# Kernel tuning notes

Hardware: AMD Instinct MI355X
Metric: run time of the kernel (lower is better)

## Reference

```python
import jax, jax.numpy as jnp
import numpy as np

N, E, F_IN, F_HID, K = 100000, 1600000, 64, 64, 6


def setup_inputs() -> dict:
    key = jax.random.key(0)
    k1, k2, k3, k4, k5 = jax.random.split(key, 5)
    x = jax.random.normal(k1, (N, F_IN), dtype=jnp.float32)
    # edges with no self-loops (PyG ChebConv removes self loops before normalization)
    src = jax.random.randint(k2, (E,), 0, N, dtype=jnp.int32)
    off = jax.random.randint(k3, (E,), 1, N, dtype=jnp.int32)
    dst = (src + off) % N
    edge_index = jnp.stack([src, dst], axis=0)
    # Glorot-ish init for the K Chebyshev weight matrices
    W = jax.random.normal(k4, (K, F_IN, F_HID), dtype=jnp.float32) * (1.0 / np.sqrt(F_IN))
    b = jax.random.normal(k5, (F_HID,), dtype=jnp.float32) * 0.01
    return {"x": x, "edge_index": edge_index, "W": W, "b": b}


def reference(x, edge_index, W, b):
    # ChebConv with sym normalization, lambda_max = 2.0 (PyG default):
    # scaled Laplacian L_hat = 2*L/lambda_max - I = -D^{-1/2} A D^{-1/2} (zero diagonal)
    row = edge_index[0].astype(jnp.int32)  # source j
    col = edge_index[1].astype(jnp.int32)  # target i
    n = x.shape[0]
    deg = jax.ops.segment_sum(jnp.ones_like(row, dtype=x.dtype), row, num_segments=n)
    dinv = jnp.where(deg > 0, jax.lax.rsqrt(deg), jnp.zeros_like(deg))
    w = -(dinv[row] * dinv[col])  # [E] edge weights of L_hat

    def prop(h):  # h: [N, F] -> L_hat @ h via gather-scale-scatter
        return jax.ops.segment_sum(w[:, None] * h[row], col, num_segments=n)

    # Chebyshev recurrence: Tx_0 = x, Tx_1 = L_hat x, Tx_k = 2 L_hat Tx_{k-1} - Tx_{k-2}
    Tx0 = x
    out = Tx0 @ W[0]
    Tx1 = prop(Tx0)
    out = out + Tx1 @ W[1]
    for k in range(2, W.shape[0]):
        Tx2 = 2.0 * prop(Tx1) - Tx0
        out = out + Tx2 @ W[k]
        Tx0, Tx1 = Tx1, Tx2
    return jax.nn.relu(out + b)
```

## Files before the change

kernel.cpp:

```cpp
#include <hip/hip_runtime.h>


constexpr int F = 64;
constexpr int SCAN_ELEMS = 1024;
constexpr int BSH = 9;
constexpr int EPB = 2048;
constexpr int PNPW = 8;

typedef __attribute__((ext_vector_type(8))) short short8;
typedef __attribute__((ext_vector_type(4))) float floatx4;

__device__ __forceinline__ unsigned short f_to_bf(float f) {
    unsigned u = __float_as_uint(f);
    u += 0x7FFFu + ((u >> 16) & 1u);
    return (unsigned short)(u >> 16);
}
__device__ __forceinline__ float bf_to_f(unsigned short s) {
    return __uint_as_float(((unsigned)s) << 16);
}
__device__ __forceinline__ float4 bf4_to_f4(ushort4 u) {
    float4 f;
    f.x = bf_to_f(u.x); f.y = bf_to_f(u.y); f.z = bf_to_f(u.z); f.w = bf_to_f(u.w);
    return f;
}

__global__ void hist2_kernel(const int* __restrict__ row, const int* __restrict__ col,
                             int* __restrict__ gcH, int* __restrict__ gcS,
                             int P, int G, int E) {
    __shared__ int hH[256], hS[256];
    const int tid = threadIdx.x, blk = blockIdx.x;
    hH[tid] = 0; hS[tid] = 0;
    __syncthreads();
    const int start = blk * EPB + tid * 8;
    if (start + 7 < E) {
        const int4 c0 = *(const int4*)(col + start);
        const int4 c1 = *(const int4*)(col + start + 4);
        const int4 r0 = *(const int4*)(row + start);
        const int4 r1 = *(const int4*)(row + start + 4);
        atomicAdd(&hH[c0.x >> BSH], 1); atomicAdd(&hH[c0.y >> BSH], 1);
        atomicAdd(&hH[c0.z >> BSH], 1); atomicAdd(&hH[c0.w >> BSH], 1);
        atomicAdd(&hH[c1.x >> BSH], 1); atomicAdd(&hH[c1.y >> BSH], 1);
        atomicAdd(&hH[c1.z >> BSH], 1); atomicAdd(&hH[c1.w >> BSH], 1);
        atomicAdd(&hS[r0.x >> BSH], 1); atomicAdd(&hS[r0.y >> BSH], 1);
        atomicAdd(&hS[r0.z >> BSH], 1); atomicAdd(&hS[r0.w >> BSH], 1);
        atomicAdd(&hS[r1.x >> BSH], 1); atomicAdd(&hS[r1.y >> BSH], 1);
        atomicAdd(&hS[r1.z >> BSH], 1); atomicAdd(&hS[r1.w >> BSH], 1);
    } else {
        for (int k = start; k < E && k < start + 8; ++k) {
            atomicAdd(&hH[col[k] >> BSH], 1);
            atomicAdd(&hS[row[k] >> BSH], 1);
        }
    }
    __syncthreads();
    if (tid < P) {
        gcH[(size_t)tid * G + blk] = hH[tid];
        gcS[(size_t)tid * G + blk] = hS[tid];
    }
}

__device__ __forceinline__ int4 load_cnt4(const int* __restrict__ cnt, int i, int N) {
    int4 v = make_int4(0, 0, 0, 0);
    if (i + 3 < N) {
        v = *(const int4*)(cnt + i);
    } else {
        if (i + 0 < N) v.x = cnt[i + 0];
        if (i + 1 < N) v.y = cnt[i + 1];
        if (i + 2 < N) v.z = cnt[i + 2];
        if (i + 3 < N) v.w = cnt[i + 3];
    }
    return v;
}

__global__ void scan1_kernel(const int* __restrict__ cnt, int* __restrict__ bsum, int N) {
    const int tid = threadIdx.x;
    const int i = blockIdx.x * SCAN_ELEMS + tid * 4;
    int4 v = load_cnt4(cnt, i, N);
    int s = v.x + v.y + v.z + v.w;
#pragma unroll
    for (int off = 1; off < 64; off <<= 1) s += __shfl_xor(s, off);
    __shared__ int ws[4];
    if ((tid & 63) == 0) ws[tid >> 6] = s;
    __syncthreads();
    if (tid == 0) bsum[blockIdx.x] = ws[0] + ws[1] + ws[2] + ws[3];
}

__global__ void scan2_kernel(const int* __restrict__ bsum, int* __restrict__ boff,
                             int* __restrict__ total_out, int nb) {
    const int tid = threadIdx.x;
    const int lane = tid & 63, w = tid >> 6;
    int v = (tid < nb) ? bsum[tid] : 0;
    int inc = v;
#pragma unroll
    for (int off = 1; off < 64; off <<= 1) {
        int t = __shfl_up(inc, off);
        if (lane >= off) inc += t;
    }
    __shared__ int wsum[4];
    if (lane == 63) wsum[w] = inc;
    __syncthreads();
    int wo = 0;
    for (int k = 0; k < w; ++k) wo += wsum[k];
    const int excl = wo + inc - v;
    if (tid < nb) boff[tid] = excl;
    if (tid == nb - 1) *total_out = excl + v;
}

__global__ void scan3_kernel(const int* __restrict__ cnt, const int* __restrict__ boff,
                             int* __restrict__ dst, int N) {
    const int tid = threadIdx.x;
    const int lane = tid & 63, w = tid >> 6;
    const int i = blockIdx.x * SCAN_ELEMS + tid * 4;
    int4 v = load_cnt4(cnt, i, N);
    const int s = v.x + v.y + v.z + v.w;
    int inc = s;
#pragma unroll
    for (int off = 1; off < 64; off <<= 1) {
        int t = __shfl_up(inc, off);
        if (lane >= off) inc += t;
    }
    __shared__ int wsum[4];
    if (lane == 63) wsum[w] = inc;
    __syncthreads();
    int wo = 0;
    for (int k = 0; k < w; ++k) wo += wsum[k];
    const int r0 = boff[blockIdx.x] + wo + inc - s;
    const int r1 = r0 + v.x, r2 = r1 + v.y, r3 = r2 + v.z;
    if (i + 3 < N) {
        *(int4*)(dst + i) = make_int4(r0, r1, r2, r3);
    } else {
        if (i + 0 < N) dst[i + 0] = r0;
        if (i + 1 < N) dst[i + 1] = r1;
        if (i + 2 < N) dst[i + 2] = r2;
        if (i + 3 < N) dst[i + 3] = r3;
    }
}

__global__ void part2_kernel(const int* __restrict__ row, const int* __restrict__ col,
                             const int* __restrict__ goH, const int* __restrict__ goS,
                             int2* __restrict__ partH, int* __restrict__ partS,
                             int P, int G, int E) {
    __shared__ int cH[256], cS[256];
    const int tid = threadIdx.x, blk = blockIdx.x;
    if (tid < P) {
        cH[tid] = goH[(size_t)tid * G + blk];
        cS[tid] = goS[(size_t)tid * G + blk];
    }
    __syncthreads();
    const int start = blk * EPB + tid * 8;
    for (int k = start; k < E && k < start + 8; ++k) {
        const int c = col[k], r = row[k];
        const int posH = atomicAdd(&cH[c >> BSH], 1);
        partH[posH] = make_int2(c, r);
        const int posS = atomicAdd(&cS[r >> BSH], 1);
        partS[posS] = r;
    }
}

__global__ void bucketC_kernel(const int2* __restrict__ part, const int* __restrict__ goff,
                               int* __restrict__ rowptr, int* __restrict__ csr,
                               int P, int G, int N, int E) {
    __shared__ int cnt[512];
    __shared__ int excl[512];
    __shared__ int wsum[4];
    const int tid = threadIdx.x;
    const int b = blockIdx.x;
    const int base_node = b << BSH;
    const int nn = min(512, N - base_node);
    const int estart = goff[(size_t)b * G];
    const int eend = (b + 1 < P) ? goff[(size_t)(b + 1) * G] : E;

    cnt[tid] = 0; cnt[tid + 256] = 0;
    __syncthreads();
    for (int i = estart + tid; i < eend; i += 256)
        atomicAdd(&cnt[part[i].x - base_node], 1);
    __syncthreads();
    {
        const int lane = tid & 63, w = tid >> 6;
        const int a0 = cnt[2 * tid], a1 = cnt[2 * tid + 1];
        const int ps = a0 + a1;
        int inc = ps;
#pragma unroll
        for (int off = 1; off < 64; off <<= 1) {
            int t = __shfl_up(inc, off);
            if (lane >= off) inc += t;
        }
        if (lane == 63) wsum[w] = inc;
        __syncthreads();
        int wo = 0;
        for (int k = 0; k < w; ++k) wo += wsum[k];
        const int ep = wo + inc - ps;
        excl[2 * tid] = ep;
        excl[2 * tid + 1] = ep + a0;
    }
    __syncthreads();
    if (tid < nn) rowptr[base_node + tid] = estart + excl[tid];
    for (int ln = 256 + tid; ln < nn; ln += 256) rowptr[base_node + ln] = estart + excl[ln];
    if (b == P - 1 && tid == 0) rowptr[N] = E;
    cnt[tid] = 0; cnt[tid + 256] = 0;
    __syncthreads();
    for (int i = estart + tid; i < eend; i += 256) {
        const int2 e = part[i];
        const int ln = e.x - base_node;
        const int pos = atomicAdd(&cnt[ln], 1);
        csr[estart + excl[ln] + pos] = e.y;
    }
}

__global__ void bucketD_kernel(const int* __restrict__ partS, const int* __restrict__ goffS,
                               float* __restrict__ dinv, float* __restrict__ dinv2,
                               float* __restrict__ rdinv, int P, int G, int N, int E) {
    __shared__ int cnt[512];
    const int tid = threadIdx.x;
    const int b = blockIdx.x;
    const int base_node = b << BSH;
    const int nn = min(512, N - base_node);
    const int estart = goffS[(size_t)b * G];
    const int eend = (b + 1 < P) ? goffS[(size_t)(b + 1) * G] : E;
    cnt[tid] = 0; cnt[tid + 256] = 0;
    __syncthreads();
    for (int i = estart + tid; i < eend; i += 256)
        atomicAdd(&cnt[partS[i] - base_node], 1);
    __syncthreads();
    for (int l = tid; l < nn; l += 256) {
        const int dI = cnt[l];
        const float d = (float)dI;
        const bool ok = dI > 0;
        dinv[base_node + l]  = ok ? rsqrtf(d) : 0.0f;
        dinv2[base_node + l] = ok ? 1.0f / d : 0.0f;
        rdinv[base_node + l] = ok ? sqrtf(d) : 0.0f;
    }
}

__global__ void init_s0_kernel(const float* __restrict__ dinv, const float* __restrict__ x,
                               unsigned short* __restrict__ S0b, int NF) {
    int i = blockIdx.x * blockDim.x + threadIdx.x;
    int j = i * 4;
    if (j >= NF) return;
    const float dv = dinv[j >> 6];
    const float4 v = *(const float4*)(x + j);
    ushort4 u;
    u.x = f_to_bf(dv * v.x); u.y = f_to_bf(dv * v.y);
    u.z = f_to_bf(dv * v.z); u.w = f_to_bf(dv * v.w);
    *(ushort4*)(S0b + j) = u;
}

template <int FIRST>
__global__ __launch_bounds__(256, 8)
void prop_g4(const int* __restrict__ rowptr, const int* __restrict__ csr,
             const float* __restrict__ dinv2, const unsigned short* __restrict__ Sprev,
             const unsigned short* __restrict__ Sm2, unsigned short* __restrict__ Sk, int N) {
    const int lane = threadIdx.x & 63;
    const int g16 = lane & 48;
    const int fl = lane & 15;
    const int wave = threadIdx.x >> 6;
    const int nwaves = blockDim.x >> 6;
    const int wbase = (blockIdx.x * nwaves + wave) * PNPW;
    for (int j = 0; j < PNPW; j += 4) {
        const int n = wbase + j + (g16 >> 4);
        const bool nv = n < N;
        const int nc = nv ? n : N - 1;
        const int s = rowptr[nc];
        const int e = rowptr[nc + 1];
        const int len = e - s;
        float4 acc = {0.f, 0.f, 0.f, 0.f};
        for (int c = 0; c < len; c += 16) {
            const int ii = s + c + fl;
            const int idxv = csr[ii < e ? ii : e - 1];
            const int mm = min(16, len - c);
            for (int jj = 0; jj < mm; jj += 4) {
                const int i0 = __shfl(idxv, g16 + jj + 0);
                const int i1 = __shfl(idxv, g16 + jj + 1);
                const int i2 = __shfl(idxv, g16 + jj + 2);
                const int i3 = __shfl(idxv, g16 + jj + 3);
                const ushort4 u0 = *(const ushort4*)(Sprev + (size_t)i0 * F + fl * 4);
                const ushort4 u1 = *(const ushort4*)(Sprev + (size_t)i1 * F + fl * 4);
                const ushort4 u2 = *(const ushort4*)(Sprev + (size_t)i2 * F + fl * 4);
                const ushort4 u3 = *(const ushort4*)(Sprev + (size_t)i3 * F + fl * 4);
                {
                    const float4 v = bf4_to_f4(u0);
                    acc.x += v.x; acc.y += v.y; acc.z += v.z; acc.w += v.w;
                }
                if (jj + 1 < mm) {
                    const float4 v = bf4_to_f4(u1);
                    acc.x += v.x; acc.y += v.y; acc.z += v.z; acc.w += v.w;
                }
                if (jj + 2 < mm) {
                    const float4 v = bf4_to_f4(u2);
                    acc.x += v.x; acc.y += v.y; acc.z += v.z; acc.w += v.w;
                }
                if (jj + 3 < mm) {
                    const float4 v = bf4_to_f4(u3);
                    acc.x += v.x; acc.y += v.y; acc.z += v.z; acc.w += v.w;
                }
            }
        }
        if (nv) {
            const float d2 = dinv2[n];
            float4 sn;
            if (FIRST) {
                sn.x = -d2 * acc.x; sn.y = -d2 * acc.y;
                sn.z = -d2 * acc.z; sn.w = -d2 * acc.w;
            } else {
                const float4 m2 = bf4_to_f4(*(const ushort4*)(Sm2 + (size_t)n * F + fl * 4));
                sn.x = -2.f * d2 * acc.x - m2.x; sn.y = -2.f * d2 * acc.y - m2.y;
                sn.z = -2.f * d2 * acc.z - m2.z; sn.w = -2.f * d2 * acc.w - m2.w;
            }
            ushort4 o;
            o.x = f_to_bf(sn.x); o.y = f_to_bf(sn.y);
            o.z = f_to_bf(sn.z); o.w = f_to_bf(sn.w);
            *(ushort4*)(Sk + (size_t)n * F + fl * 4) = o;
        }
    }
}

__global__ void wfrag_kernel(const float* __restrict__ W, unsigned short* __restrict__ Wfrag) {
    const int idx = blockIdx.x * blockDim.x + threadIdx.x;
    if (idx >= 4 * 12 * 64) return;
    const int lane = idx & 63;
    const int s = (idx >> 6) % 12;
    const int ft = idx / (64 * 12);
    const int n = ft * 16 + (lane & 15);
    const int quad = lane >> 4;
    unsigned short v[8];
#pragma unroll
    for (int j = 0; j < 8; ++j) {
        const int kg = s * 32 + quad * 8 + j;
        const int kk = kg >> 6, f = kg & 63;
        v[j] = f_to_bf(W[kk * F * F + f * F + n]);
    }
    ushort4 lo = {v[0], v[1], v[2], v[3]};
    ushort4 hi = {v[4], v[5], v[6], v[7]};
    *(ushort4*)(Wfrag + (size_t)idx * 8) = lo;
    *(ushort4*)(Wfrag + (size_t)idx * 8 + 4) = hi;
}

__global__ __launch_bounds__(256, 4)
void mfma_out_kernel(const float* __restrict__ x, const unsigned short* __restrict__ Sstack,
                     const unsigned short* __restrict__ Wfrag, const float* __restrict__ rdinv,
                     const float* __restrict__ dinv2, const float* __restrict__ W,
                     const float* __restrict__ b, float* __restrict__ out, int N, int NF) {
    const int lane = threadIdx.x & 63;
    const int wave = threadIdx.x >> 6;
    const int quad = lane >> 4;
    const int tm = blockIdx.x * 16;
    const int ma = tm + (lane & 15);
    const int mac = ma < N ? ma : N - 1;

    floatx4 C0 = {0.f, 0.f, 0.f, 0.f};
    floatx4 C1 = {0.f, 0.f, 0.f, 0.f};
    const unsigned short* wf = Wfrag + ((size_t)(wave * 12) * 64 + lane) * 8;

    {
        const float* xr = x + (size_t)mac * F + quad * 8;
#pragma unroll
        for (int s = 0; s < 2; ++s) {
            const float4 a0 = *(const float4*)(xr + s * 32);
            const float4 a1 = *(const float4*)(xr + s * 32 + 4);
            short8 A;
            A[0] = (short)f_to_bf(a0.x); A[1] = (short)f_to_bf(a0.y);
            A[2] = (short)f_to_bf(a0.z); A[3] = (short)f_to_bf(a0.w);
            A[4] = (short)f_to_bf(a1.x); A[5] = (short)f_to_bf(a1.y);
            A[6] = (short)f_to_bf(a1.z); A[7] = (short)f_to_bf(a1.w);
            const short8 B = *(const short8*)(wf + (size_t)s * 64 * 8);
            C0 = __builtin_amdgcn_mfma_f32_16x16x32_bf16(A, B, C0, 0, 0, 0);
        }
    }
#pragma unroll
    for (int s = 2; s < 12; ++s) {
        const int kk = s >> 1, f0 = (s & 1) * 32;
        const short8 A = *(const short8*)(Sstack + (size_t)kk * NF + (size_t)mac * F + f0 + quad * 8);
        const short8 B = *(const short8*)(wf + (size_t)s * 64 * 8);
        C1 = __builtin_amdgcn_mfma_f32_16x16x32_bf16(A, B, C1, 0, 0, 0);
    }

    const int n = wave * 16 + (lane & 15);
    const float bl = b[n];
#pragma unroll
    for (int r = 0; r < 4; ++r) {
        const int m = tm + quad * 4 + r;
        if (m >= N) continue;
        float v = C0[r] + rdinv[m] * C1[r];
        if (dinv2[m] == 0.0f) {
            const float* xr = x + (size_t)m * F;
            float fx = 0.f;
            for (int f = 0; f < F; ++f)
                fx += xr[f] * (W[4 * F * F + f * F + n] - W[2 * F * F + f * F + n]);
            v += fx;
        }
        out[(size_t)m * F + n] = fmaxf(v + bl, 0.f);
    }
}

extern "C" void kernel_launch(void* const* d_in, const int* in_sizes, int n_in,
                              void* d_out, int out_size, void* d_ws, size_t ws_size,
                              hipStream_t stream) {
    const float* x = (const float*)d_in[0];
    const int* ei = (const int*)d_in[1];
    const float* W = (const float*)d_in[2];
    const float* b = (const float*)d_in[3];

    const int N = in_sizes[0] / F;
    const int E = in_sizes[1] / 2;
    const int NF = N * F;
    const int* row = ei;
    const int* col = ei + E;

    const int P = (N + 511) >> BSH;
    const int G = (E + EPB - 1) / EPB;
    const int M = P * G;

    char* p = (char*)d_ws;
    auto alloc = [&](size_t bytes) {
        char* r = p;
        p += (bytes + 63) & ~(size_t)63;
        return r;
    };
    float* dinv   = (float*)alloc((size_t)N * sizeof(float));
    float* dinv2  = (float*)alloc((size_t)N * sizeof(float));
    float* rdinv  = (float*)alloc((size_t)N * sizeof(float));
    int*   rowptr = (int*)alloc((size_t)(N + 1) * sizeof(int));
    int*   bsum   = (int*)alloc(256 * sizeof(int));
    int*   boff   = (int*)alloc(256 * sizeof(int));
    int*   totS   = (int*)alloc(64);
    int*   gcH    = (int*)alloc((size_t)M * sizeof(int));
    int*   goH    = (int*)alloc((size_t)M * sizeof(int));
    int*   gcS    = (int*)alloc((size_t)M * sizeof(int));
    int*   goS    = (int*)alloc((size_t)M * sizeof(int));
    int*   csr    = (int*)alloc((size_t)E * sizeof(int));
    unsigned short* Sstack = (unsigned short*)alloc((size_t)6 * NF * sizeof(unsigned short));
    unsigned short* Wfrag  = (unsigned short*)alloc((size_t)4 * 12 * 64 * 8 * sizeof(unsigned short));
    int2* partH = (int2*)Sstack;
    int*  partS = (int*)(Sstack + (size_t)NF);
    float* out = (float*)d_out;

    const int B = 256;
    const int nsbM = (M + SCAN_ELEMS - 1) / SCAN_ELEMS;
    const int pgrid = (N + 4 * PNPW - 1) / (4 * PNPW);

    hist2_kernel<<<G, B, 0, stream>>>(row, col, gcH, gcS, P, G, E);
    scan1_kernel<<<nsbM, B, 0, stream>>>(gcH, bsum, M);
    scan2_kernel<<<1, B, 0, stream>>>(bsum, boff, rowptr + N, nsbM);
    scan3_kernel<<<nsbM, B, 0, stream>>>(gcH, boff, goH, M);
    scan1_kernel<<<nsbM, B, 0, stream>>>(gcS, bsum, M);
    scan2_kernel<<<1, B, 0, stream>>>(bsum, boff, totS, nsbM);
    scan3_kernel<<<nsbM, B, 0, stream>>>(gcS, boff, goS, M);
    part2_kernel<<<G, B, 0, stream>>>(row, col, goH, goS, partH, partS, P, G, E);
    bucketC_kernel<<<P, B, 0, stream>>>(partH, goH, rowptr, csr, P, G, N, E);
    bucketD_kernel<<<P, B, 0, stream>>>(partS, goS, dinv, dinv2, rdinv, P, G, N, E);

    wfrag_kernel<<<(4 * 12 * 64 + B - 1) / B, B, 0, stream>>>(W, Wfrag);
    init_s0_kernel<<<(NF / 4 + B - 1) / B, B, 0, stream>>>(dinv, x, Sstack, NF);
    prop_g4<1><<<pgrid, B, 0, stream>>>(rowptr, csr, dinv2, Sstack, Sstack,
                                        Sstack + (size_t)1 * NF, N);
    for (int k = 2; k < 6; ++k) {
        prop_g4<0><<<pgrid, B, 0, stream>>>(
            rowptr, csr, dinv2, Sstack + (size_t)(k - 1) * NF,
            Sstack + (size_t)(k - 2) * NF, Sstack + (size_t)k * NF, N);
    }
    mfma_out_kernel<<<(N + 15) / 16, 256, 0, stream>>>(x, Sstack, Wfrag, rdinv, dinv2,
                                                       W, b, out, N, NF);
}
```

Baseline: 397.8 us.

## Gather neighbor features in FP8 during Chebyshev propagation, merge output MFMA loop

```diff
diff --git a/kernel.cpp b/kernel.cpp
--- a/kernel.cpp
+++ b/kernel.cpp
@@ -9,6 +9,16 @@
 
 typedef __attribute__((ext_vector_type(8))) short short8;
 typedef __attribute__((ext_vector_type(4))) float floatx4;
+typedef __attribute__((ext_vector_type(2))) float floatx2;
+
+#if defined(__has_builtin)
+#if __has_builtin(__builtin_amdgcn_cvt_pk_f32_fp8) && __has_builtin(__builtin_amdgcn_cvt_pk_fp8_f32)
+#define HAVE_FP8 1
+#endif
+#endif
+#ifndef HAVE_FP8
+#define HAVE_FP8 0
+#endif
 
 __device__ __forceinline__ unsigned short f_to_bf(float f) {
     unsigned u = __float_as_uint(f);
@@ -23,6 +33,25 @@
     f.x = bf_to_f(u.x); f.y = bf_to_f(u.y); f.z = bf_to_f(u.z); f.w = bf_to_f(u.w);
     return f;
 }
+
+#if HAVE_FP8
+__device__ __forceinline__ float4 fp8x4_to_f4(unsigned u) {
+    floatx2 lo = __builtin_amdgcn_cvt_pk_f32_fp8((int)u, false);
+    floatx2 hi = __builtin_amdgcn_cvt_pk_f32_fp8((int)u, true);
+    float4 f;
+    f.x = lo.x; f.y = lo.y; f.z = hi.x; f.w = hi.y;
+    return f;
+}
+__device__ __forceinline__ unsigned f4_to_fp8x4(float a, float b, float c, float d) {
+    int pk = 0;
+    pk = __builtin_amdgcn_cvt_pk_fp8_f32(a, b, pk, false);
+    pk = __builtin_amdgcn_cvt_pk_fp8_f32(c, d, pk, true);
+    return (unsigned)pk;
+}
+#else
+__device__ __forceinline__ float4 fp8x4_to_f4(unsigned u) { return make_float4(0, 0, 0, 0); }
+__device__ __forceinline__ unsigned f4_to_fp8x4(float a, float b, float c, float d) { return 0; }
+#endif
 
 __global__ void hist2_kernel(const int* __restrict__ row, const int* __restrict__ col,
                              int* __restrict__ gcH, int* __restrict__ gcS,
@@ -232,16 +261,18 @@
 }
 
 __global__ void init_s0_kernel(const float* __restrict__ dinv, const float* __restrict__ x,
-                               unsigned short* __restrict__ S0b, int NF) {
+                               unsigned short* __restrict__ S0b, unsigned char* __restrict__ S0f8,
+                               int NF, int write8) {
     int i = blockIdx.x * blockDim.x + threadIdx.x;
     int j = i * 4;
     if (j >= NF) return;
     const float dv = dinv[j >> 6];
     const float4 v = *(const float4*)(x + j);
+    const float a = dv * v.x, bb = dv * v.y, c = dv * v.z, d = dv * v.w;
     ushort4 u;
-    u.x = f_to_bf(dv * v.x); u.y = f_to_bf(dv * v.y);
-    u.z = f_to_bf(dv * v.z); u.w = f_to_bf(dv * v.w);
+    u.x = f_to_bf(a); u.y = f_to_bf(bb); u.z = f_to_bf(c); u.w = f_to_bf(d);
     *(ushort4*)(S0b + j) = u;
+    if (write8) *(unsigned*)(S0f8 + j) = f4_to_fp8x4(a, bb, c, d);
 }
 
 template <int FIRST>
@@ -253,14 +284,12 @@
     const int g16 = lane & 48;
     const int fl = lane & 15;
     const int wave = threadIdx.x >> 6;
-    const int nwaves = blockDim.x >> 6;
-    const int wbase = (blockIdx.x * nwaves + wave) * PNPW;
+    const int wbase = (blockIdx.x * 4 + wave) * PNPW;
     for (int j = 0; j < PNPW; j += 4) {
         const int n = wbase + j + (g16 >> 4);
         const bool nv = n < N;
         const int nc = nv ? n : N - 1;
-        const int s = rowptr[nc];
-        const int e = rowptr[nc + 1];
+        const int s = rowptr[nc], e = rowptr[nc + 1];
         const int len = e - s;
         float4 acc = {0.f, 0.f, 0.f, 0.f};
         for (int c = 0; c < len; c += 16) {
@@ -313,6 +342,75 @@
     }
 }
 
+template <int FIRST, int W8>
+__global__ __launch_bounds__(256, 8)
+void prop_f8(const int* __restrict__ rowptr, const int* __restrict__ csr,
+             const float* __restrict__ dinv2, const unsigned char* __restrict__ S8prev,
+             const unsigned short* __restrict__ Sm2, unsigned short* __restrict__ Sk,
+             unsigned char* __restrict__ Sk8, int N) {
+    const int lane = threadIdx.x & 63;
+    const int g16 = lane & 48;
+    const int fl = lane & 15;
+    const int wave = threadIdx.x >> 6;
+    const int wbase = (blockIdx.x * 4 + wave) * PNPW;
+    for (int j = 0; j < PNPW; j += 4) {
+        const int n = wbase + j + (g16 >> 4);
+        const bool nv = n < N;
+        const int nc = nv ? n : N - 1;
+        const int s = rowptr[nc], e = rowptr[nc + 1];
+        const int len = e - s;
+        float4 acc = {0.f, 0.f, 0.f, 0.f};
+        for (int c = 0; c < len; c += 16) {
+            const int ii = s + c + fl;
+            const int idxv = csr[ii < e ? ii : e - 1];
+            const int mm = min(16, len - c);
+            for (int jj = 0; jj < mm; jj += 4) {
+                const int i0 = __shfl(idxv, g16 + jj + 0);
+                const int i1 = __shfl(idxv, g16 + jj + 1);
+                const int i2 = __shfl(idxv, g16 + jj + 2);
+                const int i3 = __shfl(idxv, g16 + jj + 3);
+                const unsigned u0 = *(const unsigned*)(S8prev + (size_t)i0 * F + fl * 4);
+                const unsigned u1 = *(const unsigned*)(S8prev + (size_t)i1 * F + fl * 4);
+                const unsigned u2 = *(const unsigned*)(S8prev + (size_t)i2 * F + fl * 4);
+                const unsigned u3 = *(const unsigned*)(S8prev + (size_t)i3 * F + fl * 4);
+                {
+                    const float4 v = fp8x4_to_f4(u0);
+                    acc.x += v.x; acc.y += v.y; acc.z += v.z; acc.w += v.w;
+                }
+                if (jj + 1 < mm) {
+                    const float4 v = fp8x4_to_f4(u1);
+                    acc.x += v.x; acc.y += v.y; acc.z += v.z; acc.w += v.w;
+                }
+                if (jj + 2 < mm) {
+                    const float4 v = fp8x4_to_f4(u2);
+                    acc.x += v.x; acc.y += v.y; acc.z += v.z; acc.w += v.w;
+                }
+                if (jj + 3 < mm) {
+                    const float4 v = fp8x4_to_f4(u3);
+                    acc.x += v.x; acc.y += v.y; acc.z += v.z; acc.w += v.w;
+                }
+            }
+        }
+        if (nv) {
+            const float d2 = dinv2[n];
+            float4 sn;
+            if (FIRST) {
+                sn.x = -d2 * acc.x; sn.y = -d2 * acc.y;
+                sn.z = -d2 * acc.z; sn.w = -d2 * acc.w;
+            } else {
+                const float4 m2 = bf4_to_f4(*(const ushort4*)(Sm2 + (size_t)n * F + fl * 4));
+                sn.x = -2.f * d2 * acc.x - m2.x; sn.y = -2.f * d2 * acc.y - m2.y;
+                sn.z = -2.f * d2 * acc.z - m2.z; sn.w = -2.f * d2 * acc.w - m2.w;
+            }
+            ushort4 o;
+            o.x = f_to_bf(sn.x); o.y = f_to_bf(sn.y);
+            o.z = f_to_bf(sn.z); o.w = f_to_bf(sn.w);
+            *(ushort4*)(Sk + (size_t)n * F + fl * 4) = o;
+            if (W8) *(unsigned*)(Sk8 + (size_t)n * F + fl * 4) = f4_to_fp8x4(sn.x, sn.y, sn.z, sn.w);
+        }
+    }
+}
+
 __global__ void wfrag_kernel(const float* __restrict__ W, unsigned short* __restrict__ Wfrag) {
     const int idx = blockIdx.x * blockDim.x + threadIdx.x;
     if (idx >= 4 * 12 * 64) return;
@@ -346,31 +444,16 @@
     const int ma = tm + (lane & 15);
     const int mac = ma < N ? ma : N - 1;
 
-    floatx4 C0 = {0.f, 0.f, 0.f, 0.f};
-    floatx4 C1 = {0.f, 0.f, 0.f, 0.f};
+    floatx4 C = {0.f, 0.f, 0.f, 0.f};
     const unsigned short* wf = Wfrag + ((size_t)(wave * 12) * 64 + lane) * 8;
-
-    {
-        const float* xr = x + (size_t)mac * F + quad * 8;
-#pragma unroll
-        for (int s = 0; s < 2; ++s) {
-            const float4 a0 = *(const float4*)(xr + s * 32);
-            const float4 a1 = *(const float4*)(xr + s * 32 + 4);
-            short8 A;
-            A[0] = (short)f_to_bf(a0.x); A[1] = (short)f_to_bf(a0.y);
-            A[2] = (short)f_to_bf(a0.z); A[3] = (short)f_to_bf(a0.w);
-            A[4] = (short)f_to_bf(a1.x); A[5] = (short)f_to_bf(a1.y);
-            A[6] = (short)f_to_bf(a1.z); A[7] = (short)f_to_bf(a1.w);
-            const short8 B = *(const short8*)(wf + (size_t)s * 64 * 8);
-            C0 = __builtin_amdgcn_mfma_f32_16x16x32_bf16(A, B, C0, 0, 0, 0);
-        }
-    }
-#pragma unroll
-    for (int s = 2; s < 12; ++s) {
+    const unsigned short* sa = Sstack + (size_t)mac * F + quad * 8;
+
+#pragma unroll
+    for (int s = 0; s < 12; ++s) {
         const int kk = s >> 1, f0 = (s & 1) * 32;
-        const short8 A = *(const short8*)(Sstack + (size_t)kk * NF + (size_t)mac * F + f0 + quad * 8);
+        const short8 A = *(const short8*)(sa + (size_t)kk * NF + f0);
         const short8 B = *(const short8*)(wf + (size_t)s * 64 * 8);
-        C1 = __builtin_amdgcn_mfma_f32_16x16x32_bf16(A, B, C1, 0, 0, 0);
+        C = __builtin_amdgcn_mfma_f32_16x16x32_bf16(A, B, C, 0, 0, 0);
     }
 
     const int n = wave * 16 + (lane & 15);
@@ -379,13 +462,14 @@
     for (int r = 0; r < 4; ++r) {
         const int m = tm + quad * 4 + r;
         if (m >= N) continue;
-        float v = C0[r] + rdinv[m] * C1[r];
+        float v = rdinv[m] * C[r];
         if (dinv2[m] == 0.0f) {
             const float* xr = x + (size_t)m * F;
             float fx = 0.f;
             for (int f = 0; f < F; ++f)
-                fx += xr[f] * (W[4 * F * F + f * F + n] - W[2 * F * F + f * F + n]);
-            v += fx;
+                fx += xr[f] * (W[0 * F * F + f * F + n] - W[2 * F * F + f * F + n] +
+                               W[4 * F * F + f * F + n]);
+            v = fx;
         }
         out[(size_t)m * F + n] = fmaxf(v + bl, 0.f);
     }
@@ -429,6 +513,10 @@
     int*   csr    = (int*)alloc((size_t)E * sizeof(int));
     unsigned short* Sstack = (unsigned short*)alloc((size_t)6 * NF * sizeof(unsigned short));
     unsigned short* Wfrag  = (unsigned short*)alloc((size_t)4 * 12 * 64 * 8 * sizeof(unsigned short));
+    unsigned char* F8A = (unsigned char*)alloc((size_t)NF);
+    unsigned char* F8B = (unsigned char*)alloc((size_t)NF);
+    const size_t needed = (size_t)(p - (char*)d_ws);
+    const bool pathA = HAVE_FP8 && ws_size >= needed;
     int2* partH = (int2*)Sstack;
     int*  partS = (int*)(Sstack + (size_t)NF);
     float* out = (float*)d_out;
@@ -449,13 +537,25 @@
     bucketD_kernel<<<P, B, 0, stream>>>(partS, goS, dinv, dinv2, rdinv, P, G, N, E);
 
     wfrag_kernel<<<(4 * 12 * 64 + B - 1) / B, B, 0, stream>>>(W, Wfrag);
-    init_s0_kernel<<<(NF / 4 + B - 1) / B, B, 0, stream>>>(dinv, x, Sstack, NF);
-    prop_g4<1><<<pgrid, B, 0, stream>>>(rowptr, csr, dinv2, Sstack, Sstack,
-                                        Sstack + (size_t)1 * NF, N);
-    for (int k = 2; k < 6; ++k) {
-        prop_g4<0><<<pgrid, B, 0, stream>>>(
-            rowptr, csr, dinv2, Sstack + (size_t)(k - 1) * NF,
-            Sstack + (size_t)(k - 2) * NF, Sstack + (size_t)k * NF, N);
+    init_s0_kernel<<<(NF / 4 + B - 1) / B, B, 0, stream>>>(dinv, x, Sstack, F8A, NF,
+                                                           pathA ? 1 : 0);
+    unsigned short* S1 = Sstack + (size_t)1 * NF;
+    unsigned short* S2 = Sstack + (size_t)2 * NF;
+    unsigned short* S3 = Sstack + (size_t)3 * NF;
+    unsigned short* S4 = Sstack + (size_t)4 * NF;
+    unsigned short* S5 = Sstack + (size_t)5 * NF;
+    if (pathA) {
+        prop_f8<1, 1><<<pgrid, B, 0, stream>>>(rowptr, csr, dinv2, F8A, Sstack, S1, F8B, N);
+        prop_f8<0, 1><<<pgrid, B, 0, stream>>>(rowptr, csr, dinv2, F8B, Sstack, S2, F8A, N);
+        prop_f8<0, 1><<<pgrid, B, 0, stream>>>(rowptr, csr, dinv2, F8A, S1, S3, F8B, N);
+        prop_f8<0, 1><<<pgrid, B, 0, stream>>>(rowptr, csr, dinv2, F8B, S2, S4, F8A, N);
+        prop_f8<0, 0><<<pgrid, B, 0, stream>>>(rowptr, csr, dinv2, F8A, S3, S5, F8B, N);
+    } else {
+        prop_g4<1><<<pgrid, B, 0, stream>>>(rowptr, csr, dinv2, Sstack, Sstack, S1, N);
+        prop_g4<0><<<pgrid, B, 0, stream>>>(rowptr, csr, dinv2, S1, Sstack, S2, N);
+        prop_g4<0><<<pgrid, B, 0, stream>>>(rowptr, csr, dinv2, S2, S1, S3, N);
+        prop_g4<0><<<pgrid, B, 0, stream>>>(rowptr, csr, dinv2, S3, S2, S4, N);
+        prop_g4<0><<<pgrid, B, 0, stream>>>(rowptr, csr, dinv2, S4, S3, S5, N);
     }
     mfma_out_kernel<<<(N + 15) / 16, 256, 0, stream>>>(x, Sstack, Wfrag, rdinv, dinv2,
                                                        W, b, out, N, NF);
```

Result: no change. 397.7 us (-0.0%).
